# Performance work log

Measured on AMD Instinct MI355X. Metric: run time of the kernel, lower is better.

The kernel has to match this reference:

```python
import jax, jax.numpy as jnp
import numpy as np

EPS = 1e-4
HEADS = 8
DIM_HEAD = 32
BALANCE = 0.3


def _normalize(x, dims):
    # torch normalize(): norm over `dims` in fp32; norm = eps + norm*sqrt(norm.numel()/x.numel())
    red = 1
    for d in dims:
        red *= x.shape[d]
    norm = jnp.sqrt(jnp.sum(jnp.square(x.astype(jnp.float32)), axis=dims, keepdims=True))
    norm = EPS + norm / np.sqrt(red)
    return x / norm.astype(x.dtype)


def _mpconv1x1(x, w, gain=1.0):
    # MPConv forward (eval mode): weight-normalize per output channel, scale, 1x1 conv
    w = w.astype(jnp.float32)
    w = _normalize(w, (1, 2, 3))
    fan_in = w.shape[1] * w.shape[2] * w.shape[3]
    w = (w * (gain / np.sqrt(fan_in))).astype(x.dtype)[:, :, 0, 0]  # [out, in]
    return jnp.einsum('oi,nihw->nohw', w, x)


def setup_inputs() -> dict:
    key = jax.random.key(0)
    k1, k2, k3 = jax.random.split(key, 3)
    x = jax.random.normal(k1, (2, 256, 48, 48), dtype=jnp.float32)
    w_qkv = jax.random.normal(k2, (768, 256, 1, 1), dtype=jnp.float32)
    w_out = jax.random.normal(k3, (256, 256, 1, 1), dtype=jnp.float32)
    return {"x": x, "w_qkv": w_qkv, "w_out": w_out}


def reference(x, w_qkv, w_out):
    n, c, h, w_sp = x.shape
    seq = h * w_sp
    y = _mpconv1x1(x, w_qkv)                          # [n, 3c, h, w]
    y = y.reshape(n, HEADS, DIM_HEAD, 3, seq)         # channel split: head x dim_head x 3
    y = _normalize(y, (2,))                           # L2-normalize over dim_head axis
    q = y[:, :, :, 0, :]
    k = y[:, :, :, 1, :]
    v = y[:, :, :, 2, :]
    # scores [n, h, q, k] with k scaled by 1/sqrt(dim_head)
    att = jax.nn.softmax(jnp.einsum('nhcq,nhck->nhqk', q, k) / np.sqrt(DIM_HEAD), axis=3)
    y = jnp.einsum('nhqk,nhck->nhcq', att, v)         # [n, heads, dim_head, seq]
    y = _mpconv1x1(y.reshape(n, c, h, w_sp), w_out)
    t = BALANCE
    # mp_sum: lerp then magnitude-preserving rescale
    return (x + t * (y - x)) / np.sqrt((1 - t) ** 2 + t ** 2)
```

## Files before the change

kernel.cpp:

```cpp
#include <hip/hip_runtime.h>
#include <math.h>

#define EPSN 1e-4f
#define SEQ 2304

using bf16x8 = __attribute__((ext_vector_type(8))) short;
using f32x4  = __attribute__((ext_vector_type(4))) float;

__device__ inline unsigned short f2bf(float x) {
    union { float f; unsigned u; } c; c.f = x;
    unsigned u = c.u;
    u += 0x7fffu + ((u >> 16) & 1u);
    return (unsigned short)(u >> 16);
}

__device__ inline unsigned cvt_pk_bf16(float lo, float hi) {
    unsigned r;
    asm("v_cvt_pk_bf16_f32 %0, %1, %2" : "=v"(r) : "v"(lo), "v"(hi));
    return r;
}
__device__ inline void permlane32_swap(unsigned &a, unsigned &b) {
    asm("v_permlane32_swap_b32 %0, %1" : "+v"(a), "+v"(b));
}
__device__ inline void permlane16_swap(unsigned &a, unsigned &b) {
    asm("v_permlane16_swap_b32 %0, %1" : "+v"(a), "+v"(b));
}

__global__ __launch_bounds__(256) void prep_kernel(const float* __restrict__ w_qkv,
                                                   const float* __restrict__ w_out,
                                                   const float* __restrict__ x,
                                                   unsigned short* __restrict__ wqb,
                                                   unsigned short* __restrict__ wob,
                                                   unsigned short* __restrict__ xt) {
    __shared__ __align__(16) unsigned short T[64][80];
    int bid = blockIdx.x;
    if (bid < 256) {
        int wave = threadIdx.x >> 6, lane = threadIdx.x & 63;
        int row = bid * 4 + wave;
        const float* src;
        unsigned short* dst;
        if (row < 768) { src = w_qkv + (size_t)row * 256; dst = wqb + (size_t)row * 256; }
        else           { src = w_out + (size_t)(row - 768) * 256; dst = wob + (size_t)(row - 768) * 256; }
        float4 v = *(const float4*)&src[lane * 4];
        float ss = v.x * v.x + v.y * v.y + v.z * v.z + v.w * v.w;
        for (int off = 32; off > 0; off >>= 1) ss += __shfl_xor(ss, off, 64);
        float sc = 1.0f / (sqrtf(ss) + 16.0f * EPSN);
        unsigned p0 = (unsigned)f2bf(v.x * sc) | ((unsigned)f2bf(v.y * sc) << 16);
        unsigned p1 = (unsigned)f2bf(v.z * sc) | ((unsigned)f2bf(v.w * sc) << 16);
        *(uint2*)&dst[lane * 4] = make_uint2(p0, p1);
    } else {
        int e0 = bid - 256;
        int st = e0 % 36, ct = (e0 / 36) & 3, n = e0 / 144;
        int t = threadIdx.x;
#pragma unroll
        for (int p = 0; p < 4; ++p) {
            int e = t + p * 256;
            int c = e >> 4, sv = (e & 15) * 4;
            float4 v = *(const float4*)&x[(size_t)(n * 256 + ct * 64 + c) * SEQ + st * 64 + sv];
            T[sv + 0][c] = f2bf(v.x);
            T[sv + 1][c] = f2bf(v.y);
            T[sv + 2][c] = f2bf(v.z);
            T[sv + 3][c] = f2bf(v.w);
        }
        __syncthreads();
#pragma unroll
        for (int p = 0; p < 2; ++p) {
            int e = t + p * 256;
            int s = e >> 3, cb = (e & 7) * 8;
            uint4 v = *(const uint4*)&T[s][cb];
            *(uint4*)&xt[(size_t)(n * SEQ + st * 64 + s) * 256 + ct * 64 + cb] = v;
        }
    }
}

__global__ __launch_bounds__(256) void qkv_fused_kernel(const unsigned short* __restrict__ xt,
                                                        const unsigned short* __restrict__ wqb,
                                                        unsigned short* __restrict__ qn,
                                                        unsigned short* __restrict__ kn,
                                                        unsigned short* __restrict__ vn) {
    __shared__ float Cs[96][65];
    __shared__ __align__(16) unsigned short Vls[32][72];
    int bid = blockIdx.x;
    int xcd = bid & 7, j = bid >> 3;
    int h = j & 7;
    int tilej = xcd * 9 + (j >> 3);
    int st = tilej % 36, n = tilej / 36;
    int tid = threadIdx.x;
    int wave = tid >> 6, lane = tid & 63;
    int ln = lane & 15, quad = lane >> 4;
    const unsigned short* Abase = wqb + (size_t)(h * 96 + ln) * 256 + quad * 8;
    const unsigned short* Bbase = xt + (size_t)(n * SEQ + st * 64 + wave * 16 + ln) * 256 + quad * 8;
    f32x4 acc[6];
#pragma unroll
    for (int m = 0; m < 6; ++m) acc[m] = (f32x4){0.f, 0.f, 0.f, 0.f};
#pragma unroll
    for (int kc = 0; kc < 8; ++kc) {
        bf16x8 b = *(const bf16x8*)(Bbase + kc * 32);
#pragma unroll
        for (int m = 0; m < 6; ++m) {
            bf16x8 a = *(const bf16x8*)(Abase + (size_t)(m * 16) * 256 + kc * 32);
            acc[m] = __builtin_amdgcn_mfma_f32_16x16x32_bf16(a, b, acc[m], 0, 0, 0);
        }
    }
#pragma unroll
    for (int m = 0; m < 6; ++m)
#pragma unroll
        for (int r = 0; r < 4; ++r)
            Cs[m * 16 + quad * 4 + r][wave * 16 + ln] = acc[m][r];
    __syncthreads();
    int nh = n * 8 + h;
    if (tid < 192) {
        int sl = tid & 63, wh = tid >> 6;
        int s = st * 64 + sl;
        float v[32];
        float ss = 0.f;
#pragma unroll
        for (int d = 0; d < 32; ++d) { v[d] = Cs[3 * d + wh][sl]; ss += v[d] * v[d]; }
        float inv = 1.0f / (EPSN + sqrtf(ss * (1.0f / 32.0f)));
        if (wh == 0) inv *= 0.17677669529663687f * 1.4426950408889634f;
        if (wh == 2) {
#pragma unroll
            for (int d = 0; d < 32; ++d) Vls[d][sl] = f2bf(v[d] * inv);
        } else {
            unsigned short* dst = (wh == 1 ? kn : qn) + (size_t)nh * 73728 + (size_t)s * 32;
            unsigned wbuf[16];
#pragma unroll
            for (int j2 = 0; j2 < 16; ++j2)
                wbuf[j2] = (unsigned)f2bf(v[2 * j2] * inv) | ((unsigned)f2bf(v[2 * j2 + 1] * inv) << 16);
#pragma unroll
            for (int j2 = 0; j2 < 4; ++j2) {
                uint4 t4 = make_uint4(wbuf[4 * j2], wbuf[4 * j2 + 1], wbuf[4 * j2 + 2], wbuf[4 * j2 + 3]);
                *(uint4*)(dst + j2 * 8) = t4;
            }
        }
    }
    __syncthreads();
    {
        int d = tid >> 3, sj = (tid & 7) * 8;
        uint4 t4 = *(const uint4*)&Vls[d][sj];
        *(uint4*)&vn[(size_t)nh * 73728 + (size_t)d * SEQ + st * 64 + sj] = t4;
    }
}

__global__ __launch_bounds__(512) void attn_mfma_kernel(const unsigned short* __restrict__ qn,
                                                        const unsigned short* __restrict__ kn,
                                                        const unsigned short* __restrict__ vn,
                                                        unsigned short* __restrict__ y2t) {
    __shared__ __align__(16) unsigned char SM[38912];
    unsigned short (*Ks)[64][40] = (unsigned short (*)[64][40])SM;
    unsigned short (*Vs)[32][72] = (unsigned short (*)[32][72])(SM + 20480);
    int tid = threadIdx.x;
    int wave = tid >> 6, lane = tid & 63;
    int ln = lane & 15, quad = lane >> 4;
    int kg = wave >> 2, wq = wave & 3;
    int bid = blockIdx.x;
    int xcd = bid & 7, bi = bid >> 3;
    int nh = xcd * 2 + (bi >= 36);
    int qt = (bi >= 36) ? bi - 36 : bi;
    int n = nh >> 3, h = nh & 7;
    const unsigned short* Qg = qn + (size_t)nh * 73728;
    const unsigned short* Kg = kn + (size_t)nh * 73728;
    const unsigned short* Vg = vn + (size_t)nh * 73728;

    bf16x8 qf = *(const bf16x8*)(Qg + (size_t)(qt * 64 + wq * 16 + ln) * 32 + quad * 8);

    f32x4 o0 = {0.f, 0.f, 0.f, 0.f};
    f32x4 o1 = {0.f, 0.f, 0.f, 0.f};
    float lsum = 0.f;

    int ts = tid & 255;
    int kg2 = kg * 2;
    int s0 = kg * 18 * 64;

    auto compute_tile = [&](int bsel) {
        const f32x4 zero = {0.f, 0.f, 0.f, 0.f};
        unsigned w[4][2];
#pragma unroll
        for (int c = 0; c < 4; ++c) {
            bf16x8 kf = *(const bf16x8*)(&Ks[bsel][c * 16 + ln][quad * 8]);
            f32x4 sc = __builtin_amdgcn_mfma_f32_16x16x32_bf16(kf, qf, zero, 0, 0, 0);
            float e0 = exp2f(sc[0]), e1 = exp2f(sc[1]);
            float e2 = exp2f(sc[2]), e3 = exp2f(sc[3]);
            lsum += (e0 + e1) + (e2 + e3);
            w[c][0] = cvt_pk_bf16(e0, e1);
            w[c][1] = cvt_pk_bf16(e2, e3);
        }
#pragma unroll
        for (int kc = 0; kc < 2; ++kc) {
            unsigned a0 = w[2 * kc][0], b0 = w[2 * kc + 1][0];
            permlane32_swap(a0, b0);
            permlane16_swap(a0, b0);
            unsigned a1 = w[2 * kc][1], b1 = w[2 * kc + 1][1];
            permlane32_swap(a1, b1);
            permlane16_swap(a1, b1);
            union { unsigned u[4]; bf16x8 v8; } pk;
            pk.u[0] = a0; pk.u[1] = a1; pk.u[2] = b0; pk.u[3] = b1;
            bf16x8 v0 = *(const bf16x8*)(&Vs[bsel][ln][kc * 32 + quad * 8]);
            bf16x8 v1 = *(const bf16x8*)(&Vs[bsel][16 + ln][kc * 32 + quad * 8]);
            o0 = __builtin_amdgcn_mfma_f32_16x16x32_bf16(pk.v8, v0, o0, 0, 0, 0);
            o1 = __builtin_amdgcn_mfma_f32_16x16x32_bf16(pk.v8, v1, o1, 0, 0, 0);
        }
    };

    uint4 kA = *(const uint4*)(Kg + (size_t)s0 * 32 + ts * 8);
    uint4 vA = *(const uint4*)(Vg + (size_t)(ts >> 3) * SEQ + s0 + (ts & 7) * 8);
    *(uint4*)(&Ks[kg2][ts >> 2][(ts & 3) * 8]) = kA;
    *(uint4*)(&Vs[kg2][ts >> 3][(ts & 7) * 8]) = vA;
    uint4 kB = *(const uint4*)(Kg + (size_t)(s0 + 64) * 32 + ts * 8);
    uint4 vB = *(const uint4*)(Vg + (size_t)(ts >> 3) * SEQ + (s0 + 64) + (ts & 7) * 8);

    for (int i = 0; i < 18; i += 2) {
        if (i + 2 < 18) {
            int sn = s0 + (i + 2) * 64;
            kA = *(const uint4*)(Kg + (size_t)sn * 32 + ts * 8);
            vA = *(const uint4*)(Vg + (size_t)(ts >> 3) * SEQ + sn + (ts & 7) * 8);
        }
        __syncthreads();
        compute_tile(kg2);
        *(uint4*)(&Ks[kg2 + 1][ts >> 2][(ts & 3) * 8]) = kB;
        *(uint4*)(&Vs[kg2 + 1][ts >> 3][(ts & 7) * 8]) = vB;
        if (i + 3 < 18) {
            int sn = s0 + (i + 3) * 64;
            kB = *(const uint4*)(Kg + (size_t)sn * 32 + ts * 8);
            vB = *(const uint4*)(Vg + (size_t)(ts >> 3) * SEQ + sn + (ts & 7) * 8);
        }
        __syncthreads();
        compute_tile(kg2 + 1);
        if (i + 2 < 18) {
            *(uint4*)(&Ks[kg2][ts >> 2][(ts & 3) * 8]) = kA;
            *(uint4*)(&Vs[kg2][ts >> 3][(ts & 7) * 8]) = vA;
        }
    }

    lsum += __shfl_xor(lsum, 16, 64);
    lsum += __shfl_xor(lsum, 32, 64);

    __syncthreads();
    float (*Os)[36] = (float (*)[36])SM;
    float* Ls = (float*)(SM + 128 * 36 * 4);
#pragma unroll
    for (int r = 0; r < 4; ++r) {
        int q = wq * 16 + quad * 4 + r;
        Os[kg * 64 + q][ln] = o0[r];
        Os[kg * 64 + q][16 + ln] = o1[r];
    }
    if (quad == 0) Ls[kg * 64 + wq * 16 + ln] = lsum;
    __syncthreads();
    {
        int q = tid >> 3, dg = (tid & 7) * 4;
        float inv = 1.0f / (Ls[q] + Ls[64 + q]);
        float r0 = (Os[q][dg + 0] + Os[64 + q][dg + 0]) * inv;
        float r1 = (Os[q][dg + 1] + Os[64 + q][dg + 1]) * inv;
        float r2 = (Os[q][dg + 2] + Os[64 + q][dg + 2]) * inv;
        float r3 = (Os[q][dg + 3] + Os[64 + q][dg + 3]) * inv;
        *(uint2*)&y2t[((size_t)(n * SEQ) + qt * 64 + q) * 256 + h * 32 + dg] =
            make_uint2(cvt_pk_bf16(r0, r1), cvt_pk_bf16(r2, r3));
    }
}

__global__ __launch_bounds__(256) void out_gemm_kernel(const unsigned short* __restrict__ y2t,
                                                       const unsigned short* __restrict__ wob,
                                                       const float* __restrict__ x,
                                                       float* __restrict__ out) {
    int st = blockIdx.x;
    int mt = blockIdx.y;
    int n  = blockIdx.z;
    int tid = threadIdx.x;
    int wave = tid >> 6, lane = tid & 63;
    int ln = lane & 15, quad = lane >> 4;
    int m0 = mt * 64 + wave * 16;
    const unsigned short* Abase = wob + (size_t)(m0 + ln) * 256 + quad * 8;
    const unsigned short* Bbase = y2t + (size_t)(n * SEQ + st * 32 + ln) * 256 + quad * 8;
    f32x4 acc[2];
#pragma unroll
    for (int c = 0; c < 2; ++c) acc[c] = (f32x4){0.f, 0.f, 0.f, 0.f};
#pragma unroll
    for (int kc = 0; kc < 8; ++kc) {
        bf16x8 a = *(const bf16x8*)(Abase + kc * 32);
#pragma unroll
        for (int c = 0; c < 2; ++c) {
            bf16x8 b = *(const bf16x8*)(Bbase + (size_t)(c * 16) * 256 + kc * 32);
            acc[c] = __builtin_amdgcn_mfma_f32_16x16x32_bf16(a, b, acc[c], 0, 0, 0);
        }
    }
    const float c0f = 0.7f * 1.3130643285972254f;
    const float c1f = 0.3f * 1.3130643285972254f;
#pragma unroll
    for (int c = 0; c < 2; ++c)
#pragma unroll
        for (int r = 0; r < 4; ++r) {
            int o = m0 + quad * 4 + r;
            int s = st * 32 + c * 16 + ln;
            size_t idx = (size_t)(n * 256 + o) * SEQ + s;
            out[idx] = c0f * x[idx] + c1f * acc[c][r];
        }
}

extern "C" void kernel_launch(void* const* d_in, const int* in_sizes, int n_in,
                              void* d_out, int out_size, void* d_ws, size_t ws_size,
                              hipStream_t stream) {
    (void)in_sizes; (void)n_in; (void)out_size; (void)ws_size;
    const float* x     = (const float*)d_in[0];
    const float* w_qkv = (const float*)d_in[1];
    const float* w_out = (const float*)d_in[2];
    float* out = (float*)d_out;
    float* ws  = (float*)d_ws;
    unsigned short* wqb = (unsigned short*)(ws);
    unsigned short* wob = (unsigned short*)(ws + 98304);
    unsigned short* xt  = (unsigned short*)(ws + 131072);
    unsigned short* y2t = (unsigned short*)(ws + 131072);
    unsigned short* qn  = (unsigned short*)(ws + 720896);
    unsigned short* kn  = (unsigned short*)(ws + 1310720);
    unsigned short* vn  = (unsigned short*)(ws + 1900544);

    hipLaunchKernelGGL(prep_kernel, dim3(544), dim3(256), 0, stream,
                       w_qkv, w_out, x, wqb, wob, xt);
    hipLaunchKernelGGL(qkv_fused_kernel, dim3(576), dim3(256), 0, stream,
                       xt, wqb, qn, kn, vn);
    hipLaunchKernelGGL(attn_mfma_kernel, dim3(576), dim3(512), 0, stream,
                       qn, kn, vn, y2t);
    hipLaunchKernelGGL(out_gemm_kernel, dim3(72, 4, 2), dim3(256), 0, stream,
                       y2t, wob, x, out);
}
```

Baseline: 134.8 us.

## Split attention key range across blocks with separate reduce kernel; smaller prep tiles

The attention kernel previously split the key range across two wave groups inside one 512-thread block and combined them through shared memory. It now launches twice as many 256-thread blocks, each covering half the keys. Each block writes fp32 partial outputs and row sums to workspace, and a new reduce kernel combines them into bf16. The row-sum is now computed with an extra MFMA against a ones vector instead of scalar adds. The x-transpose in prep uses smaller 16-sequence tiles with more blocks. This trades extra global traffic and a fifth kernel launch for more parallel blocks and fewer VALU ops.

```diff
diff --git a/kernel.cpp b/kernel.cpp
--- a/kernel.cpp
+++ b/kernel.cpp
@@ -32,7 +32,7 @@
                                                    unsigned short* __restrict__ wqb,
                                                    unsigned short* __restrict__ wob,
                                                    unsigned short* __restrict__ xt) {
-    __shared__ __align__(16) unsigned short T[64][80];
+    __shared__ __align__(16) unsigned short T[16][72];
     int bid = blockIdx.x;
     if (bid < 256) {
         int wave = threadIdx.x >> 6, lane = threadIdx.x & 63;
@@ -50,26 +50,22 @@
         *(uint2*)&dst[lane * 4] = make_uint2(p0, p1);
     } else {
         int e0 = bid - 256;
-        int st = e0 % 36, ct = (e0 / 36) & 3, n = e0 / 144;
-        int t = threadIdx.x;
-#pragma unroll
-        for (int p = 0; p < 4; ++p) {
-            int e = t + p * 256;
-            int c = e >> 4, sv = (e & 15) * 4;
-            float4 v = *(const float4*)&x[(size_t)(n * 256 + ct * 64 + c) * SEQ + st * 64 + sv];
-            T[sv + 0][c] = f2bf(v.x);
-            T[sv + 1][c] = f2bf(v.y);
-            T[sv + 2][c] = f2bf(v.z);
-            T[sv + 3][c] = f2bf(v.w);
-        }
+        int n = e0 / 576;
+        int r = e0 % 576;
+        int ct = r / 144;
+        int r2 = r % 144;
+        int st = r2 >> 2, sq = r2 & 3;
+        int tid = threadIdx.x;
+        int c = tid >> 2, sv = (tid & 3) * 4;
+        float4 v = *(const float4*)&x[(size_t)(n * 256 + ct * 64 + c) * SEQ + st * 64 + sq * 16 + sv];
+        T[sv + 0][c] = f2bf(v.x);
+        T[sv + 1][c] = f2bf(v.y);
+        T[sv + 2][c] = f2bf(v.z);
+        T[sv + 3][c] = f2bf(v.w);
         __syncthreads();
-#pragma unroll
-        for (int p = 0; p < 2; ++p) {
-            int e = t + p * 256;
-            int s = e >> 3, cb = (e & 7) * 8;
-            uint4 v = *(const uint4*)&T[s][cb];
-            *(uint4*)&xt[(size_t)(n * SEQ + st * 64 + s) * 256 + ct * 64 + cb] = v;
-        }
+        int s = tid >> 4, cb = (tid & 15) * 4;
+        uint2 t2 = *(const uint2*)&T[s][cb];
+        *(uint2*)&xt[(size_t)(n * SEQ + st * 64 + sq * 16 + s) * 256 + ct * 64 + cb] = t2;
     }
 }
 
@@ -142,35 +138,35 @@
     }
 }
 
-__global__ __launch_bounds__(512) void attn_mfma_kernel(const unsigned short* __restrict__ qn,
+__global__ __launch_bounds__(256) void attn_mfma_kernel(const unsigned short* __restrict__ qn,
                                                         const unsigned short* __restrict__ kn,
                                                         const unsigned short* __restrict__ vn,
-                                                        unsigned short* __restrict__ y2t) {
-    __shared__ __align__(16) unsigned char SM[38912];
-    unsigned short (*Ks)[64][40] = (unsigned short (*)[64][40])SM;
-    unsigned short (*Vs)[32][72] = (unsigned short (*)[32][72])(SM + 20480);
+                                                        float* __restrict__ Opart,
+                                                        float* __restrict__ Lpart) {
+    __shared__ __align__(16) unsigned short Ks[2][64][40];
+    __shared__ __align__(16) unsigned short Vs[2][32][72];
     int tid = threadIdx.x;
-    int wave = tid >> 6, lane = tid & 63;
+    int wq = tid >> 6, lane = tid & 63;
     int ln = lane & 15, quad = lane >> 4;
-    int kg = wave >> 2, wq = wave & 3;
     int bid = blockIdx.x;
     int xcd = bid & 7, bi = bid >> 3;
-    int nh = xcd * 2 + (bi >= 36);
-    int qt = (bi >= 36) ? bi - 36 : bi;
-    int n = nh >> 3, h = nh & 7;
+    int nh = xcd * 2 + (bi >= 72);
+    int bi2 = (bi >= 72) ? bi - 72 : bi;
+    int qt = bi2 % 36, kz = bi2 / 36;
     const unsigned short* Qg = qn + (size_t)nh * 73728;
     const unsigned short* Kg = kn + (size_t)nh * 73728;
     const unsigned short* Vg = vn + (size_t)nh * 73728;
 
     bf16x8 qf = *(const bf16x8*)(Qg + (size_t)(qt * 64 + wq * 16 + ln) * 32 + quad * 8);
+    bf16x8 ones;
+#pragma unroll
+    for (int i = 0; i < 8; ++i) ones[i] = (short)0x3F80;
 
     f32x4 o0 = {0.f, 0.f, 0.f, 0.f};
     f32x4 o1 = {0.f, 0.f, 0.f, 0.f};
-    float lsum = 0.f;
-
-    int ts = tid & 255;
-    int kg2 = kg * 2;
-    int s0 = kg * 18 * 64;
+    f32x4 lac = {0.f, 0.f, 0.f, 0.f};
+
+    int s0 = kz * 18 * 64;
 
     auto compute_tile = [&](int bsel) {
         const f32x4 zero = {0.f, 0.f, 0.f, 0.f};
@@ -179,11 +175,8 @@
         for (int c = 0; c < 4; ++c) {
             bf16x8 kf = *(const bf16x8*)(&Ks[bsel][c * 16 + ln][quad * 8]);
             f32x4 sc = __builtin_amdgcn_mfma_f32_16x16x32_bf16(kf, qf, zero, 0, 0, 0);
-            float e0 = exp2f(sc[0]), e1 = exp2f(sc[1]);
-            float e2 = exp2f(sc[2]), e3 = exp2f(sc[3]);
-            lsum += (e0 + e1) + (e2 + e3);
-            w[c][0] = cvt_pk_bf16(e0, e1);
-            w[c][1] = cvt_pk_bf16(e2, e3);
+            w[c][0] = cvt_pk_bf16(exp2f(sc[0]), exp2f(sc[1]));
+            w[c][1] = cvt_pk_bf16(exp2f(sc[2]), exp2f(sc[3]));
         }
 #pragma unroll
         for (int kc = 0; kc < 2; ++kc) {
@@ -197,63 +190,75 @@
             pk.u[0] = a0; pk.u[1] = a1; pk.u[2] = b0; pk.u[3] = b1;
             bf16x8 v0 = *(const bf16x8*)(&Vs[bsel][ln][kc * 32 + quad * 8]);
             bf16x8 v1 = *(const bf16x8*)(&Vs[bsel][16 + ln][kc * 32 + quad * 8]);
-            o0 = __builtin_amdgcn_mfma_f32_16x16x32_bf16(pk.v8, v0, o0, 0, 0, 0);
-            o1 = __builtin_amdgcn_mfma_f32_16x16x32_bf16(pk.v8, v1, o1, 0, 0, 0);
+            lac = __builtin_amdgcn_mfma_f32_16x16x32_bf16(pk.v8, ones, lac, 0, 0, 0);
+            o0  = __builtin_amdgcn_mfma_f32_16x16x32_bf16(pk.v8, v0, o0, 0, 0, 0);
+            o1  = __builtin_amdgcn_mfma_f32_16x16x32_bf16(pk.v8, v1, o1, 0, 0, 0);
         }
     };
 
-    uint4 kA = *(const uint4*)(Kg + (size_t)s0 * 32 + ts * 8);
-    uint4 vA = *(const uint4*)(Vg + (size_t)(ts >> 3) * SEQ + s0 + (ts & 7) * 8);
-    *(uint4*)(&Ks[kg2][ts >> 2][(ts & 3) * 8]) = kA;
-    *(uint4*)(&Vs[kg2][ts >> 3][(ts & 7) * 8]) = vA;
-    uint4 kB = *(const uint4*)(Kg + (size_t)(s0 + 64) * 32 + ts * 8);
-    uint4 vB = *(const uint4*)(Vg + (size_t)(ts >> 3) * SEQ + (s0 + 64) + (ts & 7) * 8);
+    uint4 kA = *(const uint4*)(Kg + (size_t)s0 * 32 + tid * 8);
+    uint4 vA = *(const uint4*)(Vg + (size_t)(tid >> 3) * SEQ + s0 + (tid & 7) * 8);
+    *(uint4*)(&Ks[0][tid >> 2][(tid & 3) * 8]) = kA;
+    *(uint4*)(&Vs[0][tid >> 3][(tid & 7) * 8]) = vA;
+    uint4 kB = *(const uint4*)(Kg + (size_t)(s0 + 64) * 32 + tid * 8);
+    uint4 vB = *(const uint4*)(Vg + (size_t)(tid >> 3) * SEQ + (s0 + 64) + (tid & 7) * 8);
 
     for (int i = 0; i < 18; i += 2) {
         if (i + 2 < 18) {
             int sn = s0 + (i + 2) * 64;
-            kA = *(const uint4*)(Kg + (size_t)sn * 32 + ts * 8);
-            vA = *(const uint4*)(Vg + (size_t)(ts >> 3) * SEQ + sn + (ts & 7) * 8);
+            kA = *(const uint4*)(Kg + (size_t)sn * 32 + tid * 8);
+            vA = *(const uint4*)(Vg + (size_t)(tid >> 3) * SEQ + sn + (tid & 7) * 8);
         }
         __syncthreads();
-        compute_tile(kg2);
-        *(uint4*)(&Ks[kg2 + 1][ts >> 2][(ts & 3) * 8]) = kB;
-        *(uint4*)(&Vs[kg2 + 1][ts >> 3][(ts & 7) * 8]) = vB;
+        compute_tile(0);
+        *(uint4*)(&Ks[1][tid >> 2][(tid & 3) * 8]) = kB;
+        *(uint4*)(&Vs[1][tid >> 3][(tid & 7) * 8]) = vB;
         if (i + 3 < 18) {
             int sn = s0 + (i + 3) * 64;
-            kB = *(const uint4*)(Kg + (size_t)sn * 32 + ts * 8);
-            vB = *(const uint4*)(Vg + (size_t)(ts >> 3) * SEQ + sn + (ts & 7) * 8);
+            kB = *(const uint4*)(Kg + (size_t)sn * 32 + tid * 8);
+            vB = *(const uint4*)(Vg + (size_t)(tid >> 3) * SEQ + sn + (tid & 7) * 8);
         }
         __syncthreads();
-        compute_tile(kg2 + 1);
+        compute_tile(1);
         if (i + 2 < 18) {
-            *(uint4*)(&Ks[kg2][ts >> 2][(ts & 3) * 8]) = kA;
-            *(uint4*)(&Vs[kg2][ts >> 3][(ts & 7) * 8]) = vA;
-        }
-    }
-
-    lsum += __shfl_xor(lsum, 16, 64);
-    lsum += __shfl_xor(lsum, 32, 64);
-
-    __syncthreads();
-    float (*Os)[36] = (float (*)[36])SM;
-    float* Ls = (float*)(SM + 128 * 36 * 4);
+            *(uint4*)(&Ks[0][tid >> 2][(tid & 3) * 8]) = kA;
+            *(uint4*)(&Vs[0][tid >> 3][(tid & 7) * 8]) = vA;
+        }
+    }
+
+    float* Ob = Opart + ((size_t)(kz * 16 + nh) * 36 + qt) * 2048;
+    float* Lb = Lpart + ((size_t)(kz * 16 + nh) * 36 + qt) * 64;
 #pragma unroll
     for (int r = 0; r < 4; ++r) {
-        int q = wq * 16 + quad * 4 + r;
-        Os[kg * 64 + q][ln] = o0[r];
-        Os[kg * 64 + q][16 + ln] = o1[r];
-    }
-    if (quad == 0) Ls[kg * 64 + wq * 16 + ln] = lsum;
-    __syncthreads();
-    {
-        int q = tid >> 3, dg = (tid & 7) * 4;
-        float inv = 1.0f / (Ls[q] + Ls[64 + q]);
-        float r0 = (Os[q][dg + 0] + Os[64 + q][dg + 0]) * inv;
-        float r1 = (Os[q][dg + 1] + Os[64 + q][dg + 1]) * inv;
-        float r2 = (Os[q][dg + 2] + Os[64 + q][dg + 2]) * inv;
-        float r3 = (Os[q][dg + 3] + Os[64 + q][dg + 3]) * inv;
-        *(uint2*)&y2t[((size_t)(n * SEQ) + qt * 64 + q) * 256 + h * 32 + dg] =
+        int ql = wq * 16 + quad * 4 + r;
+        Ob[ql * 32 + ln]      = o0[r];
+        Ob[ql * 32 + 16 + ln] = o1[r];
+        if (ln == 0) Lb[ql] = lac[r];
+    }
+}
+
+__global__ __launch_bounds__(256) void attn_reduce_kernel(const float* __restrict__ Opart,
+                                                          const float* __restrict__ Lpart,
+                                                          unsigned short* __restrict__ y2t) {
+    int qt = blockIdx.x, nh = blockIdx.y;
+    int n = nh >> 3, h = nh & 7;
+    size_t s0 = (size_t)nh * 36 + qt;
+    const float* O0 = Opart + s0 * 2048;
+    const float* O1 = Opart + (s0 + 16 * 36) * 2048;
+    const float* L0 = Lpart + s0 * 64;
+    const float* L1 = Lpart + (s0 + 16 * 36) * 64;
+#pragma unroll
+    for (int p = 0; p < 2; ++p) {
+        int idx = (threadIdx.x + p * 256) * 4;
+        int q = idx >> 5, c = idx & 31;
+        float inv = 1.0f / (L0[q] + L1[q]);
+        float4 a = *(const float4*)&O0[idx];
+        float4 b = *(const float4*)&O1[idx];
+        float r0 = (a.x + b.x) * inv;
+        float r1 = (a.y + b.y) * inv;
+        float r2 = (a.z + b.z) * inv;
+        float r3 = (a.w + b.w) * inv;
+        *(uint2*)&y2t[((size_t)(n * SEQ) + qt * 64 + q) * 256 + h * 32 + c] =
             make_uint2(cvt_pk_bf16(r0, r1), cvt_pk_bf16(r2, r3));
     }
 }
@@ -312,13 +317,17 @@
     unsigned short* qn  = (unsigned short*)(ws + 720896);
     unsigned short* kn  = (unsigned short*)(ws + 1310720);
     unsigned short* vn  = (unsigned short*)(ws + 1900544);
-
-    hipLaunchKernelGGL(prep_kernel, dim3(544), dim3(256), 0, stream,
+    float* Opart = ws + 2490368;
+    float* Lpart = ws + 4849664;
+
+    hipLaunchKernelGGL(prep_kernel, dim3(1408), dim3(256), 0, stream,
                        w_qkv, w_out, x, wqb, wob, xt);
     hipLaunchKernelGGL(qkv_fused_kernel, dim3(576), dim3(256), 0, stream,
                        xt, wqb, qn, kn, vn);
-    hipLaunchKernelGGL(attn_mfma_kernel, dim3(576), dim3(512), 0, stream,
-                       qn, kn, vn, y2t);
+    hipLaunchKernelGGL(attn_mfma_kernel, dim3(1152), dim3(256), 0, stream,
+                       qn, kn, vn, Opart, Lpart);
+    hipLaunchKernelGGL(attn_reduce_kernel, dim3(36, 16), dim3(256), 0, stream,
+                       Opart, Lpart, y2t);
     hipLaunchKernelGGL(out_gemm_kernel, dim3(72, 4, 2), dim3(256), 0, stream,
                        y2t, wob, x, out);
 }
```

Result: no change. 134.7 us (-0.1%).
